# Performance work log

Hardware: AMD Instinct MI355X
Metric: run time of the kernel (lower is better)

Reference implementation:

```python
import jax, jax.numpy as jnp
import numpy as np

N_CTX = 4096
D_MODEL = 1024
D_HEAD = 64


def setup_inputs() -> dict:
    key = jax.random.key(0)
    k_x, k_q, k_k, k_o, k_v = jax.random.split(key, 5)
    return {
        "x": jax.random.normal(k_x, (N_CTX, D_MODEL), dtype=jnp.float32),
        "W_q": jax.random.normal(k_q, (D_MODEL, D_HEAD), dtype=jnp.float32),
        "W_kT": jax.random.normal(k_k, (D_HEAD, D_MODEL), dtype=jnp.float32),
        "W_o": jax.random.normal(k_o, (D_MODEL, D_HEAD), dtype=jnp.float32),
        "W_vT": jax.random.normal(k_v, (D_HEAD, D_MODEL), dtype=jnp.float32),
    }


def reference(x, W_q, W_kT, W_o, W_vT):
    # x: [n, d_model]
    n = x.shape[0]
    q = x @ W_q                      # [n, d_head]
    k = x @ W_kT.T                   # [n, d_head]  (W_kT @ x.T transposed)
    scores = q @ k.T                 # [n, n] -- NOTE: original has no 1/sqrt(d_head) scaling
    # causal mask: upper triangle (strictly above diagonal) set to -inf
    causal = jnp.tril(jnp.ones((n, n), dtype=bool))
    scores = jnp.where(causal, scores, -jnp.inf)
    attn = jax.nn.softmax(scores, axis=1)  # softmax over keys (dim=1)
    v = x @ W_o @ W_vT               # [n, d_model] -- faithful to attn @ x @ W_o @ W_vT
    return attn @ v                  # [n, d_model]
```

## Files before the change

### kernel.cpp

```cpp
#include <hip/hip_runtime.h>
#include <hip/hip_bf16.h>
#include <math.h>

#define DM    1024
#define DH    64
#define NCTX  4096
#define NCH   8

typedef __attribute__((ext_vector_type(8))) short bf16x8;
typedef __attribute__((ext_vector_type(4))) float f32x4;

#define D_QH   0
#define D_QM   524288
#define D_QL   1048576
#define D_KH   1572864
#define D_KM   2097152
#define D_KL   2621440
#define D_UTB  3145728
#define D_PY   3670016
#define D_PM   12058624
#define D_PL   12189696
#define D_WTH  12320768
#define D_WTM  12713984

#define S_YH   0
#define S_YM   524288
#define S_WVH  1048576
#define S_WVM  1179648

__device__ __forceinline__ ushort f2bf(float x) {
  __hip_bfloat16 h = __float2bfloat16(x);
  return __builtin_bit_cast(ushort, h);
}
__device__ __forceinline__ float bf2f(ushort u) {
  __hip_bfloat16 h = __builtin_bit_cast(__hip_bfloat16, u);
  return __bfloat162float(h);
}

typedef __attribute__((address_space(1))) const unsigned int gas_u32;
typedef __attribute__((address_space(3))) unsigned int las_u32;
__device__ __forceinline__ void gload_lds16(const void* g, void* l) {
  __builtin_amdgcn_global_load_lds((gas_u32*)g, (las_u32*)l, 16, 0, 0);
}

__global__ __launch_bounds__(256) void wsplit_kernel(
    const float* __restrict__ Wq, const float* __restrict__ WkT,
    const float* __restrict__ Wo, const float* __restrict__ Wv,
    ushort* __restrict__ WTh, ushort* __restrict__ WTm,
    ushort* __restrict__ WvTh, ushort* __restrict__ WvTm)
{
  int gid = blockIdx.x * 256 + threadIdx.x;
  int mat = gid >> 16;
  int idx = gid & 65535;
  if (mat == 3) {
    float v = Wv[idx];
    int h = idx >> 10, c = idx & 1023;
    int oidx = c * 64 + h;
    ushort h16 = f2bf(v);
    WvTh[oidx] = h16;
    WvTm[oidx] = f2bf(v - bf2f(h16));
    return;
  }
  float v; int oidx;
  if (mat == 1) {
    v = WkT[idx];
    oidx = 65536 + idx;
  } else {
    int k = idx >> 6, h = idx & 63;
    v = (mat == 0 ? Wq : Wo)[idx];
    oidx = mat * 65536 + h * 1024 + k;
  }
  ushort h16 = f2bf(v);
  float rem = v - bf2f(h16);
  WTh[oidx] = h16;
  WTm[oidx] = f2bf(rem);
}

__global__ __launch_bounds__(256, 2) void proj_mfma_kernel(
    const float* __restrict__ x,
    const ushort* __restrict__ WTh, const ushort* __restrict__ WTm,
    ushort* __restrict__ Qh, ushort* __restrict__ Qm, ushort* __restrict__ Ql,
    ushort* __restrict__ Kh, ushort* __restrict__ Km, ushort* __restrict__ Kl,
    ushort* __restrict__ UTb)
{
  __shared__ __align__(16) ushort xsh[32*128], xsm[32*128];
  __shared__ __align__(16) ushort wsh[2][64*128], wsm[2][64*128];

  const int tid  = threadIdx.x;
  const int lane = tid & 63;
  const int w    = tid >> 6;
  const int q16  = lane & 15;
  const int grp  = lane >> 4;
  const int r0   = blockIdx.x * 32;
  const int mat  = blockIdx.y;
  const ushort* __restrict__ wh = WTh + mat * 65536;
  const ushort* __restrict__ wm = WTm + mat * 65536;

  const int rw  = (w & 1) * 16;
  const int ct0 = (w >> 1) * 2;

  const int xrowl = tid >> 4, xslot = tid & 15;

  auto stage_w = [&](int b, int s) {
    const int kp0 = s * 128;
    #pragma unroll
    for (int u = 0; u < 4; ++u) {
      int ubase = u * 256 + w * 64;
      int unit  = ubase + lane;
      int row   = unit >> 4, slotp = unit & 15;
      int ssrc  = slotp ^ (row & 15);
      int gsrc  = row * DM + kp0 + ssrc * 8;
      gload_lds16(&wh[gsrc], &wsh[b][ubase * 8]);
      gload_lds16(&wm[gsrc], &wsm[b][ubase * 8]);
    }
  };
  auto xload = [&](int s, float4& a0, float4& a1, float4& b0, float4& b1) {
    const int kp0 = s * 128;
    const float* s0 = &x[(r0 + xrowl) * DM + kp0 + xslot * 8];
    const float* s1 = &x[(r0 + xrowl + 16) * DM + kp0 + xslot * 8];
    a0 = *(const float4*)&s0[0]; a1 = *(const float4*)&s0[4];
    b0 = *(const float4*)&s1[0]; b1 = *(const float4*)&s1[4];
  };
  auto xsplit_write = [&](float4 a0, float4 a1, float4 b0, float4 b1) {
    float xv0[8] = {a0.x,a0.y,a0.z,a0.w,a1.x,a1.y,a1.z,a1.w};
    float xv1[8] = {b0.x,b0.y,b0.z,b0.w,b1.x,b1.y,b1.z,b1.w};
    bf16x8 hv0, mv0, hv1, mv1;
    #pragma unroll
    for (int e = 0; e < 8; ++e) {
      ushort h0 = f2bf(xv0[e]);
      hv0[e] = (short)h0;  mv0[e] = (short)f2bf(xv0[e] - bf2f(h0));
      ushort h1 = f2bf(xv1[e]);
      hv1[e] = (short)h1;  mv1[e] = (short)f2bf(xv1[e] - bf2f(h1));
    }
    int d0 = xrowl * 128 + ((xslot ^ (xrowl & 15)) << 3);
    int r1 = xrowl + 16;
    int d1 = r1 * 128 + ((xslot ^ (r1 & 15)) << 3);
    *(bf16x8*)&xsh[d0] = hv0;  *(bf16x8*)&xsm[d0] = mv0;
    *(bf16x8*)&xsh[d1] = hv1;  *(bf16x8*)&xsm[d1] = mv1;
  };

  f32x4 acc[2] = {{0,0,0,0},{0,0,0,0}};

  {
    float4 a0, a1, b0, b1;
    xload(0, a0, a1, b0, b1);
    xsplit_write(a0, a1, b0, b1);
    stage_w(0, 0);
  }
  __syncthreads();

  int cur = 0;
  for (int stg = 0; stg < 8; ++stg) {
    float4 na0, na1, nb0, nb1;
    if (stg < 7) {
      xload(stg + 1, na0, na1, nb0, nb1);
      stage_w(cur ^ 1, stg + 1);
    }
    #pragma unroll
    for (int ksub = 0; ksub < 4; ++ksub) {
      const int s = ksub * 4 + grp;
      const int xrow = rw + q16;
      bf16x8 xh8 = *(const bf16x8*)&xsh[xrow * 128 + ((s ^ (xrow & 15)) << 3)];
      bf16x8 xm8 = *(const bf16x8*)&xsm[xrow * 128 + ((s ^ (xrow & 15)) << 3)];
      #pragma unroll
      for (int i = 0; i < 2; ++i) {
        const int wrow = (ct0 + i) * 16 + q16;
        const int woff = wrow * 128 + ((s ^ (wrow & 15)) << 3);
        bf16x8 bh = *(const bf16x8*)&wsh[cur][woff];
        bf16x8 bm = *(const bf16x8*)&wsm[cur][woff];
        if (mat == 2) {
          acc[i] = __builtin_amdgcn_mfma_f32_16x16x32_bf16(bh, xh8, acc[i], 0,0,0);
          acc[i] = __builtin_amdgcn_mfma_f32_16x16x32_bf16(bh, xm8, acc[i], 0,0,0);
          acc[i] = __builtin_amdgcn_mfma_f32_16x16x32_bf16(bm, xh8, acc[i], 0,0,0);
          acc[i] = __builtin_amdgcn_mfma_f32_16x16x32_bf16(bm, xm8, acc[i], 0,0,0);
        } else {
          acc[i] = __builtin_amdgcn_mfma_f32_16x16x32_bf16(xh8, bh, acc[i], 0,0,0);
          acc[i] = __builtin_amdgcn_mfma_f32_16x16x32_bf16(xh8, bm, acc[i], 0,0,0);
          acc[i] = __builtin_amdgcn_mfma_f32_16x16x32_bf16(xm8, bh, acc[i], 0,0,0);
          acc[i] = __builtin_amdgcn_mfma_f32_16x16x32_bf16(xm8, bm, acc[i], 0,0,0);
        }
      }
    }
    __syncthreads();
    if (stg < 7) xsplit_write(na0, na1, nb0, nb1);
    __syncthreads();
    cur ^= 1;
  }

  if (mat == 2) {
    #pragma unroll
    for (int i = 0; i < 2; ++i)
      #pragma unroll
      for (int r = 0; r < 4; ++r)
        UTb[((ct0 + i)*16 + 4*grp + r) * NCTX + r0 + rw + q16] = f2bf(acc[i][r]);
  } else {
    ushort* __restrict__ Dh = (mat == 0) ? Qh : Kh;
    ushort* __restrict__ Dm = (mat == 0) ? Qm : Km;
    ushort* __restrict__ Dl = (mat == 0) ? Ql : Kl;
    #pragma unroll
    for (int i = 0; i < 2; ++i)
      #pragma unroll
      for (int r = 0; r < 4; ++r) {
        float v = acc[i][r];
        ushort h = f2bf(v); float fh = bf2f(h);
        ushort m = f2bf(v - fh); float fm = bf2f(m);
        ushort l = f2bf(v - fh - fm);
        int idx = (r0 + rw + 4*grp + r) * DH + (ct0 + i)*16 + q16;
        Dh[idx] = h; Dm[idx] = m; Dl[idx] = l;
      }
  }
}

__global__ __launch_bounds__(256, 2) void attn_kernel(
    const ushort* __restrict__ Qh, const ushort* __restrict__ Qm, const ushort* __restrict__ Ql,
    const ushort* __restrict__ Kh, const ushort* __restrict__ Km, const ushort* __restrict__ Kl,
    const ushort* __restrict__ UTb,
    float* __restrict__ Pm, float* __restrict__ Pl, float* __restrict__ Py)
{
  __shared__ ushort Ksh[2][3][64*64];
  __shared__ ushort Ush[2][64*64];
  __shared__ __align__(16) ushort ps[4][16*72];

  const int tid  = threadIdx.x;
  const int lane = tid & 63;
  const int w    = tid >> 6;
  ushort* psw = ps[w];
  const int q16  = lane & 15;
  const int grp  = lane >> 4;
  const int colb = grp * 8;

  const int qq    = blockIdx.x;
  const int c     = blockIdx.y;
  const int gbase = 252 - 4 * qq;
  const int g     = gbase + w;
  const int gmax  = gbase + 3;
  const int T     = ((16*gmax + 15) >> 6) + 1;
  const int t0 = (c * T) >> 3, t1 = ((c+1) * T) >> 3;
  const int Town = ((16*g + 15) >> 6) + 1;
  const int q0 = 16 * g;
  const int q  = q0 + q16;

  auto stage = [&](int b, int t) {
    const int j0 = t * 64;
    #pragma unroll
    for (int it = 0; it < 2; ++it) {
      int ubase = it * 256 + w * 64;
      int unit  = ubase + lane;
      int row   = unit >> 3, slotp = unit & 7;
      int c8    = slotp ^ (row & 7);
      int src   = (j0 + row) * DH + c8 * 8;
      gload_lds16(&Kh[src], &Ksh[b][0][ubase * 8]);
      gload_lds16(&Km[src], &Ksh[b][1][ubase * 8]);
      gload_lds16(&Kl[src], &Ksh[b][2][ubase * 8]);
      gload_lds16(&UTb[row * NCTX + j0 + c8 * 8], &Ush[b][ubase * 8]);
    }
  };

  bf16x8 fqh[2], fqm[2], fql[2];
  #pragma unroll
  for (int ks = 0; ks < 2; ++ks) {
    int off = (q0 + q16)*DH + 32*ks + colb;
    fqh[ks] = *(const bf16x8*)&Qh[off];
    fqm[ks] = *(const bf16x8*)&Qm[off];
    fql[ks] = *(const bf16x8*)&Ql[off];
  }

  float mrun = -3.0e38f, lrun = 0.f;
  f32x4 yacc[4] = {{0,0,0,0},{0,0,0,0},{0,0,0,0},{0,0,0,0}};

  if (t0 < t1) stage(0, t0);
  __syncthreads();

  int cur = 0;
  for (int t = t0; t < t1; ++t) {
    if (t + 1 < t1) stage(cur ^ 1, t + 1);
    if (t < Town) {
      const int j0 = t * 64;
      f32x4 sa[4] = {{0,0,0,0},{0,0,0,0},{0,0,0,0},{0,0,0,0}};
      #pragma unroll
      for (int ks = 0; ks < 2; ++ks) {
        #pragma unroll
        for (int st = 0; st < 4; ++st) {
          int row = 16*st + q16;
          int off = row * 64 + (((4*ks + grp) ^ (row & 7)) << 3);
          bf16x8 kh = *(const bf16x8*)&Ksh[cur][0][off];
          bf16x8 km = *(const bf16x8*)&Ksh[cur][1][off];
          bf16x8 kl = *(const bf16x8*)&Ksh[cur][2][off];
          sa[st] = __builtin_amdgcn_mfma_f32_16x16x32_bf16(kh, fqh[ks], sa[st], 0,0,0);
          sa[st] = __builtin_amdgcn_mfma_f32_16x16x32_bf16(kh, fqm[ks], sa[st], 0,0,0);
          sa[st] = __builtin_amdgcn_mfma_f32_16x16x32_bf16(km, fqh[ks], sa[st], 0,0,0);
          sa[st] = __builtin_amdgcn_mfma_f32_16x16x32_bf16(km, fqm[ks], sa[st], 0,0,0);
          sa[st] = __builtin_amdgcn_mfma_f32_16x16x32_bf16(kh, fql[ks], sa[st], 0,0,0);
          sa[st] = __builtin_amdgcn_mfma_f32_16x16x32_bf16(kl, fqh[ks], sa[st], 0,0,0);
        }
      }
      #pragma unroll
      for (int st = 0; st < 4; ++st)
        #pragma unroll
        for (int r = 0; r < 4; ++r) {
          int key = j0 + 16*st + 4*grp + r;
          if (key > q) sa[st][r] = -3.0e38f;
        }
      float mx = sa[0][0];
      #pragma unroll
      for (int st = 0; st < 4; ++st)
        #pragma unroll
        for (int r = 0; r < 4; ++r) mx = fmaxf(mx, sa[st][r]);
      mx = fmaxf(mx, __shfl_xor(mx, 16));
      mx = fmaxf(mx, __shfl_xor(mx, 32));
      float mnew  = fmaxf(mrun, mx);
      float alpha = __expf(mrun - mnew);
      float ts = 0.f;
      ushort pb[16];
      #pragma unroll
      for (int st = 0; st < 4; ++st)
        #pragma unroll
        for (int r = 0; r < 4; ++r) {
          float p = __expf(sa[st][r] - mnew);
          ts += p;
          pb[st*4 + r] = f2bf(p);
        }
      ts += __shfl_xor(ts, 16);
      ts += __shfl_xor(ts, 32);
      lrun = lrun * alpha + ts;
      mrun = mnew;
      float ar[4];
      #pragma unroll
      for (int r = 0; r < 4; ++r) ar[r] = __shfl(alpha, 4*grp + r, 64);
      #pragma unroll
      for (int dt = 0; dt < 4; ++dt) {
        yacc[dt][0] *= ar[0]; yacc[dt][1] *= ar[1];
        yacc[dt][2] *= ar[2]; yacc[dt][3] *= ar[3];
      }
      #pragma unroll
      for (int st = 0; st < 4; ++st) {
        uint2 v;
        v.x = (uint)pb[st*4+0] | ((uint)pb[st*4+1] << 16);
        v.y = (uint)pb[st*4+2] | ((uint)pb[st*4+3] << 16);
        *(uint2*)&psw[q16*72 + 16*st + 4*grp] = v;
      }
      __threadfence_block();
      __builtin_amdgcn_sched_barrier(0);
      #pragma unroll
      for (int ks = 0; ks < 2; ++ks) {
        bf16x8 pa = *(const bf16x8*)&psw[q16*72 + 32*ks + colb];
        #pragma unroll
        for (int dt = 0; dt < 4; ++dt) {
          int row = 16*dt + q16;
          int off = row * 64 + (((4*ks + grp) ^ (row & 7)) << 3);
          bf16x8 ub = *(const bf16x8*)&Ush[cur][off];
          yacc[dt] = __builtin_amdgcn_mfma_f32_16x16x32_bf16(pa, ub, yacc[dt], 0,0,0);
        }
      }
    }
    __syncthreads();
    cur ^= 1;
  }
  if (grp == 0) {
    Pm[c * NCTX + q] = mrun;
    Pl[c * NCTX + q] = lrun;
  }
  #pragma unroll
  for (int dt = 0; dt < 4; ++dt)
    #pragma unroll
    for (int r = 0; r < 4; ++r)
      Py[(c * NCTX + q0 + 4*grp + r) * DH + 16*dt + q16] = yacc[dt][r];
}

__global__ __launch_bounds__(256) void combine_kernel(
    const float* __restrict__ Pm, const float* __restrict__ Pl,
    const float* __restrict__ Py,
    ushort* __restrict__ Yh, ushort* __restrict__ Ym)
{
  int idx = blockIdx.x * 256 + threadIdx.x;
  int r = idx >> 6, d = idx & 63;
  float mv[NCH];
  float M = -3.0e38f;
  #pragma unroll
  for (int c = 0; c < NCH; ++c) {
    mv[c] = Pm[c*NCTX + r];
    M = fmaxf(M, mv[c]);
  }
  float num = 0.f, den = 0.f;
  #pragma unroll
  for (int c = 0; c < NCH; ++c) {
    float s = __expf(mv[c] - M);
    den += s * Pl[c*NCTX + r];
    num += s * Py[(c*NCTX + r)*DH + d];
  }
  float y = num / den;
  ushort h = f2bf(y);
  Yh[idx] = h;
  Ym[idx] = f2bf(y - bf2f(h));
}

__global__ __launch_bounds__(256, 3) void out_mfma_kernel(
    const ushort* __restrict__ Yh_g, const ushort* __restrict__ Ym_g,
    const ushort* __restrict__ WvTh, const ushort* __restrict__ WvTm,
    float* __restrict__ out)
{
  __shared__ __align__(16) ushort Yh[64*64], Ym[64*64];
  __shared__ __align__(16) ushort Wsh[128*64], Wsm[128*64];

  const int tid  = threadIdx.x;
  const int lane = tid & 63;
  const int w    = tid >> 6;
  const int q16  = lane & 15;
  const int grp  = lane >> 4;
  const int r0   = blockIdx.x * 64;
  const int cb   = blockIdx.y;

  #pragma unroll
  for (int it = 0; it < 2; ++it) {
    int ubase = it * 256 + w * 64;
    int unit  = ubase + lane;
    int row   = unit >> 3, slotp = unit & 7;
    int c8    = slotp ^ (row & 7);
    int src   = (r0 + row) * 64 + c8 * 8;
    gload_lds16(&Yh_g[src], &Yh[ubase * 8]);
    gload_lds16(&Ym_g[src], &Ym[ubase * 8]);
  }
  #pragma unroll
  for (int u = 0; u < 4; ++u) {
    int ubase = u * 256 + w * 64;
    int unit  = ubase + lane;
    int row   = unit >> 3, slotp = unit & 7;
    int c8    = slotp ^ (row & 7);
    int src   = (cb * 128 + row) * 64 + c8 * 8;
    gload_lds16(&WvTh[src], &Wsh[ubase * 8]);
    gload_lds16(&WvTm[src], &Wsm[ubase * 8]);
  }
  __syncthreads();

  f32x4 acc[4][2] = {};
  #pragma unroll
  for (int ks = 0; ks < 2; ++ks) {
    bf16x8 ah[4], am[4];
    #pragma unroll
    for (int rt = 0; rt < 4; ++rt) {
      int row = 16*rt + q16;
      int off = row*64 + (((4*ks + grp) ^ (row & 7)) << 3);
      ah[rt] = *(const bf16x8*)&Yh[off];
      am[rt] = *(const bf16x8*)&Ym[off];
    }
    #pragma unroll
    for (int lt = 0; lt < 2; ++lt) {
      int crow = w*32 + lt*16 + q16;
      int off  = crow*64 + (((4*ks + grp) ^ (crow & 7)) << 3);
      bf16x8 bh = *(const bf16x8*)&Wsh[off];
      bf16x8 bm = *(const bf16x8*)&Wsm[off];
      #pragma unroll
      for (int rt = 0; rt < 4; ++rt) {
        acc[rt][lt] = __builtin_amdgcn_mfma_f32_16x16x32_bf16(ah[rt], bh, acc[rt][lt], 0,0,0);
        acc[rt][lt] = __builtin_amdgcn_mfma_f32_16x16x32_bf16(ah[rt], bm, acc[rt][lt], 0,0,0);
        acc[rt][lt] = __builtin_amdgcn_mfma_f32_16x16x32_bf16(am[rt], bh, acc[rt][lt], 0,0,0);
        acc[rt][lt] = __builtin_amdgcn_mfma_f32_16x16x32_bf16(am[rt], bm, acc[rt][lt], 0,0,0);
      }
    }
  }
  #pragma unroll
  for (int rt = 0; rt < 4; ++rt)
    #pragma unroll
    for (int lt = 0; lt < 2; ++lt)
      #pragma unroll
      for (int r = 0; r < 4; ++r)
        out[(r0 + 16*rt + 4*grp + r) * DM + cb*128 + w*32 + lt*16 + q16] = acc[rt][lt][r];
}

extern "C" void kernel_launch(void* const* d_in, const int* in_sizes, int n_in,
                              void* d_out, int out_size, void* d_ws, size_t ws_size,
                              hipStream_t stream) {
  const float* x   = (const float*)d_in[0];
  const float* Wq  = (const float*)d_in[1];
  const float* WkT = (const float*)d_in[2];
  const float* Wo  = (const float*)d_in[3];
  const float* Wv  = (const float*)d_in[4];
  float* out = (float*)d_out;
  char*  ob  = (char*)d_out;
  char*  wb  = (char*)d_ws;

  ushort* Qhp = (ushort*)(ob + D_QH);
  ushort* Qmp = (ushort*)(ob + D_QM);
  ushort* Qlp = (ushort*)(ob + D_QL);
  ushort* Khp = (ushort*)(ob + D_KH);
  ushort* Kmp = (ushort*)(ob + D_KM);
  ushort* Klp = (ushort*)(ob + D_KL);
  ushort* UTb = (ushort*)(ob + D_UTB);
  float*  Pyp = (float*)(ob + D_PY);
  float*  Pmp = (float*)(ob + D_PM);
  float*  Plp = (float*)(ob + D_PL);
  ushort* WTh = (ushort*)(ob + D_WTH);
  ushort* WTm = (ushort*)(ob + D_WTM);

  ushort* Yhp  = (ushort*)(wb + S_YH);
  ushort* Ymp  = (ushort*)(wb + S_YM);
  ushort* WvTh = (ushort*)(wb + S_WVH);
  ushort* WvTm = (ushort*)(wb + S_WVM);

  hipLaunchKernelGGL(wsplit_kernel, dim3(1024), dim3(256), 0, stream,
                     Wq, WkT, Wo, Wv, WTh, WTm, WvTh, WvTm);
  hipLaunchKernelGGL(proj_mfma_kernel, dim3(128, 3), dim3(256), 0, stream,
                     x, WTh, WTm, Qhp, Qmp, Qlp, Khp, Kmp, Klp, UTb);
  hipLaunchKernelGGL(attn_kernel, dim3(64, 8), dim3(256), 0, stream,
                     Qhp, Qmp, Qlp, Khp, Kmp, Klp, UTb, Pmp, Plp, Pyp);
  hipLaunchKernelGGL(combine_kernel, dim3(1024), dim3(256), 0, stream,
                     Pmp, Plp, Pyp, Yhp, Ymp);
  hipLaunchKernelGGL(out_mfma_kernel, dim3(64, 8), dim3(256), 0, stream,
                     Yhp, Ymp, WvTh, WvTm, out);
}
```

Measured before the change: 62.62 us.

## Fuse split-softmax combine into output projection kernel when workspace is large

Adds a fused kernel that merges the per-chunk partial softmax results (max, sum, partial outputs) and converts Y to split bf16 hi/lo in shared memory. It then runs the output projection with MFMA, removing one launch and the global round-trip for Y. The partial buffers move from the output buffer into workspace when the workspace is large enough, so the fused kernel never reads data it is overwriting in out. Each of the 8 column blocks recomputes the combine for its 64 rows, which adds redundant reads of Py.

```diff
diff --git a/kernel.cpp b/kernel.cpp
--- a/kernel.cpp
+++ b/kernel.cpp
@@ -23,10 +23,14 @@
 #define D_WTH  12320768
 #define D_WTM  12713984
 
-#define S_YH   0
-#define S_YM   524288
-#define S_WVH  1048576
-#define S_WVM  1179648
+#define S_WVH  0
+#define S_WVM  131072
+#define S_PM   262144
+#define S_PL   393216
+#define S_PY   524288
+#define S_END  8912896
+#define S_YH   262144
+#define S_YM   786432
 
 __device__ __forceinline__ ushort f2bf(float x) {
   __hip_bfloat16 h = __float2bfloat16(x);
@@ -367,6 +371,121 @@
       Py[(c * NCTX + q0 + 4*grp + r) * DH + 16*dt + q16] = yacc[dt][r];
 }
 
+__global__ __launch_bounds__(256, 3) void out_fused_kernel(
+    const float* __restrict__ Pm, const float* __restrict__ Pl,
+    const float* __restrict__ Py,
+    const ushort* __restrict__ WvTh, const ushort* __restrict__ WvTm,
+    float* __restrict__ out)
+{
+  __shared__ __align__(16) ushort Yh[64*64], Ym[64*64];
+  __shared__ __align__(16) ushort Wsh[128*64], Wsm[128*64];
+  __shared__ float sden[NCH][64];
+  __shared__ float invd[64];
+
+  const int tid  = threadIdx.x;
+  const int lane = tid & 63;
+  const int w    = tid >> 6;
+  const int q16  = lane & 15;
+  const int grp  = lane >> 4;
+  const int r0   = blockIdx.x * 64;
+  const int cb   = blockIdx.y;
+
+  #pragma unroll
+  for (int u = 0; u < 4; ++u) {
+    int ubase = u * 256 + w * 64;
+    int unit  = ubase + lane;
+    int row   = unit >> 3, slotp = unit & 7;
+    int c8    = slotp ^ (row & 7);
+    int src   = (cb * 128 + row) * 64 + c8 * 8;
+    gload_lds16(&WvTh[src], &Wsh[ubase * 8]);
+    gload_lds16(&WvTm[src], &Wsm[ubase * 8]);
+  }
+  if (tid < 64) {
+    int rrow = r0 + tid;
+    float mv[NCH]; float M = -3.0e38f;
+    #pragma unroll
+    for (int c = 0; c < NCH; ++c) {
+      mv[c] = Pm[c*NCTX + rrow];
+      M = fmaxf(M, mv[c]);
+    }
+    float den = 0.f;
+    #pragma unroll
+    for (int c = 0; c < NCH; ++c) {
+      float s = __expf(mv[c] - M);
+      sden[c][tid] = s;
+      den += s * Pl[c*NCTX + rrow];
+    }
+    invd[tid] = 1.0f / den;
+  }
+  __syncthreads();
+
+  #pragma unroll
+  for (int it = 0; it < 4; ++it) {
+    int idx = it * 256 + tid;
+    int h4 = idx & 15, rr = idx >> 4;
+    int rrow = r0 + rr;
+    float nx = 0.f, ny = 0.f, nz = 0.f, nw = 0.f;
+    #pragma unroll
+    for (int c = 0; c < NCH; ++c) {
+      float s = sden[c][rr];
+      float4 p4 = *(const float4*)&Py[(c*NCTX + rrow)*DH + h4*4];
+      nx += s*p4.x; ny += s*p4.y; nz += s*p4.z; nw += s*p4.w;
+    }
+    float inv = invd[rr];
+    float yv[4] = {nx*inv, ny*inv, nz*inv, nw*inv};
+    ushort hv[4], mv4[4];
+    #pragma unroll
+    for (int e = 0; e < 4; ++e) {
+      ushort h = f2bf(yv[e]);
+      hv[e] = h;
+      mv4[e] = f2bf(yv[e] - bf2f(h));
+    }
+    int off = rr*64 + (((h4 >> 1) ^ (rr & 7)) << 3) + (h4 & 1) * 4;
+    uint2 vh, vm;
+    vh.x = (uint)hv[0] | ((uint)hv[1] << 16);
+    vh.y = (uint)hv[2] | ((uint)hv[3] << 16);
+    vm.x = (uint)mv4[0] | ((uint)mv4[1] << 16);
+    vm.y = (uint)mv4[2] | ((uint)mv4[3] << 16);
+    *(uint2*)&Yh[off] = vh;
+    *(uint2*)&Ym[off] = vm;
+  }
+  __syncthreads();
+
+  f32x4 acc[4][2] = {};
+  #pragma unroll
+  for (int ks = 0; ks < 2; ++ks) {
+    bf16x8 ah[4], am[4];
+    #pragma unroll
+    for (int rt = 0; rt < 4; ++rt) {
+      int row = 16*rt + q16;
+      int off = row*64 + (((4*ks + grp) ^ (row & 7)) << 3);
+      ah[rt] = *(const bf16x8*)&Yh[off];
+      am[rt] = *(const bf16x8*)&Ym[off];
+    }
+    #pragma unroll
+    for (int lt = 0; lt < 2; ++lt) {
+      int crow = w*32 + lt*16 + q16;
+      int off  = crow*64 + (((4*ks + grp) ^ (crow & 7)) << 3);
+      bf16x8 bh = *(const bf16x8*)&Wsh[off];
+      bf16x8 bm = *(const bf16x8*)&Wsm[off];
+      #pragma unroll
+      for (int rt = 0; rt < 4; ++rt) {
+        acc[rt][lt] = __builtin_amdgcn_mfma_f32_16x16x32_bf16(ah[rt], bh, acc[rt][lt], 0,0,0);
+        acc[rt][lt] = __builtin_amdgcn_mfma_f32_16x16x32_bf16(ah[rt], bm, acc[rt][lt], 0,0,0);
+        acc[rt][lt] = __builtin_amdgcn_mfma_f32_16x16x32_bf16(am[rt], bh, acc[rt][lt], 0,0,0);
+        acc[rt][lt] = __builtin_amdgcn_mfma_f32_16x16x32_bf16(am[rt], bm, acc[rt][lt], 0,0,0);
+      }
+    }
+  }
+  #pragma unroll
+  for (int rt = 0; rt < 4; ++rt)
+    #pragma unroll
+    for (int lt = 0; lt < 2; ++lt)
+      #pragma unroll
+      for (int r = 0; r < 4; ++r)
+        out[(r0 + 16*rt + 4*grp + r) * DM + cb*128 + w*32 + lt*16 + q16] = acc[rt][lt][r];
+}
+
 __global__ __launch_bounds__(256) void combine_kernel(
     const float* __restrict__ Pm, const float* __restrict__ Pl,
     const float* __restrict__ Py,
@@ -486,16 +605,17 @@
   ushort* Kmp = (ushort*)(ob + D_KM);
   ushort* Klp = (ushort*)(ob + D_KL);
   ushort* UTb = (ushort*)(ob + D_UTB);
-  float*  Pyp = (float*)(ob + D_PY);
-  float*  Pmp = (float*)(ob + D_PM);
-  float*  Plp = (float*)(ob + D_PL);
   ushort* WTh = (ushort*)(ob + D_WTH);
   ushort* WTm = (ushort*)(ob + D_WTM);
 
-  ushort* Yhp  = (ushort*)(wb + S_YH);
-  ushort* Ymp  = (ushort*)(wb + S_YM);
   ushort* WvTh = (ushort*)(wb + S_WVH);
   ushort* WvTm = (ushort*)(wb + S_WVM);
+
+  const bool big_ws = (ws_size >= (size_t)S_END);
+
+  float* Pmp = big_ws ? (float*)(wb + S_PM) : (float*)(ob + D_PM);
+  float* Plp = big_ws ? (float*)(wb + S_PL) : (float*)(ob + D_PL);
+  float* Pyp = big_ws ? (float*)(wb + S_PY) : (float*)(ob + D_PY);
 
   hipLaunchKernelGGL(wsplit_kernel, dim3(1024), dim3(256), 0, stream,
                      Wq, WkT, Wo, Wv, WTh, WTm, WvTh, WvTm);
@@ -503,8 +623,15 @@
                      x, WTh, WTm, Qhp, Qmp, Qlp, Khp, Kmp, Klp, UTb);
   hipLaunchKernelGGL(attn_kernel, dim3(64, 8), dim3(256), 0, stream,
                      Qhp, Qmp, Qlp, Khp, Kmp, Klp, UTb, Pmp, Plp, Pyp);
-  hipLaunchKernelGGL(combine_kernel, dim3(1024), dim3(256), 0, stream,
-                     Pmp, Plp, Pyp, Yhp, Ymp);
-  hipLaunchKernelGGL(out_mfma_kernel, dim3(64, 8), dim3(256), 0, stream,
-                     Yhp, Ymp, WvTh, WvTm, out);
-}
+  if (big_ws) {
+    hipLaunchKernelGGL(out_fused_kernel, dim3(64, 8), dim3(256), 0, stream,
+                       Pmp, Plp, Pyp, WvTh, WvTm, out);
+  } else {
+    ushort* Yhp = (ushort*)(wb + S_YH);
+    ushort* Ymp = (ushort*)(wb + S_YM);
+    hipLaunchKernelGGL(combine_kernel, dim3(1024), dim3(256), 0, stream,
+                       Pmp, Plp, Pyp, Yhp, Ymp);
+    hipLaunchKernelGGL(out_mfma_kernel, dim3(64, 8), dim3(256), 0, stream,
+                       Yhp, Ymp, WvTh, WvTm, out);
+  }
+}
```

After: 58.48 us. 6.6% less time.
